# Performance work log

Measured on AMD Instinct MI355X. Metric: run time of the kernel, lower is better.

The kernel has to match this reference:

```python
import jax, jax.numpy as jnp
import numpy as np

V, E, HID, T, S = 50000, 512, 1024, 32, 4096
H = HID // 2  # per-direction hidden size


def setup_inputs() -> dict:
    key = jax.random.key(0)
    ks = jax.random.split(key, 16)
    f = lambda k, shape, s=0.1: (jax.random.normal(k, shape) * s).astype(jnp.float32)
    return {
        "input_ids": jax.random.randint(ks[0], (S,), 0, V),
        "target": jax.random.randint(ks[1], (S,), 0, T),
        "emb": f(ks[2], (V, E)),
        "wih_f": f(ks[3], (4 * H, E)),
        "whh_f": f(ks[4], (4 * H, H)),
        "b_f": f(ks[5], (4 * H,)),
        "wih_b": f(ks[6], (4 * H, E)),
        "whh_b": f(ks[7], (4 * H, H)),
        "b_b": f(ks[8], (4 * H,)),
        "lin_w": f(ks[9], (T, HID)),
        "lin_b": f(ks[10], (T,)),
        "start_trans": f(ks[11], (T,)),
        "end_trans": f(ks[12], (T,)),
        "trans": f(ks[13], (T, T)),
    }


def _lstm_dir(xp, whh):
    # xp: [S, 4H] precomputed input projections (x @ Wih^T + b_ih + b_hh)
    Hh = whh.shape[1]

    def step(carry, x_t):
        h, c = carry
        gates = x_t + whh @ h  # [4H]; PyTorch gate order: i, f, g, o
        i, fg, g, o = jnp.split(gates, 4)
        i = jax.nn.sigmoid(i)
        fg = jax.nn.sigmoid(fg)
        g = jnp.tanh(g)
        o = jax.nn.sigmoid(o)
        c = fg * c + i * g
        h = o * jnp.tanh(c)
        return (h, c), h

    init = (jnp.zeros((Hh,), xp.dtype), jnp.zeros((Hh,), xp.dtype))
    _, hs = jax.lax.scan(step, init, xp)
    return hs  # [S, H]


def reference(input_ids, target, emb, wih_f, whh_f, b_f, wih_b, whh_b, b_b,
              lin_w, lin_b, start_trans, end_trans, trans):
    x = emb[input_ids]  # [S, E]
    # bidirectional LSTM (batch of 1 sequence); dropout is identity (eval mode)
    h_f = _lstm_dir(x @ wih_f.T + b_f, whh_f)                # [S, H]
    h_b = _lstm_dir((x[::-1]) @ wih_b.T + b_b, whh_b)[::-1]  # [S, H]
    lstm_out = jnp.concatenate([h_f, h_b], axis=-1)          # [S, HID]
    em = lstm_out @ lin_w.T + lin_b                          # [S, T] emissions

    # CRF negative log-likelihood (mask all ones, batch=1, reduction='sum')
    idx = jnp.arange(em.shape[0])
    score = (start_trans[target[0]]
             + jnp.sum(em[idx, target])
             + jnp.sum(trans[target[:-1], target[1:]])
             + end_trans[target[-1]])

    alpha0 = start_trans + em[0]  # [T]

    def fstep(alpha, e_t):
        # logsumexp over previous tag: [T,1] + [T,T] -> [T]
        alpha = jax.scipy.special.logsumexp(alpha[:, None] + trans, axis=0) + e_t
        return alpha, None

    alpha, _ = jax.lax.scan(fstep, alpha0, em[1:])
    logZ = jax.scipy.special.logsumexp(alpha + end_trans)
    return logZ - score  # -log p(target | input), scalar
```

## Files before the change

### kernel.cpp

```cpp
#include <hip/hip_runtime.h>
#include <hip/hip_bf16.h>

#define S_LEN 4096
#define HID   512
#define E_DIM 512
#define G4    2048

__device__ __forceinline__ float fsig(float x) {
  return __fdividef(1.f, 1.f + __expf(-x));
}
__device__ __forceinline__ float ftanh_(float x) {
  return 1.f - __fdividef(2.f, __expf(2.f * x) + 1.f);
}
__device__ __forceinline__ unsigned int f2b(float f) {
  unsigned int x = __float_as_uint(f);
  return (x + 0x7FFFu + ((x >> 16) & 1u)) >> 16;
}
__device__ __forceinline__ float b2f(unsigned int b) {
  return __uint_as_float(b << 16);
}

__global__ __launch_bounds__(256) void proj_gemm(
    const int* __restrict__ ids, const float* __restrict__ emb,
    const float* __restrict__ wih_f, const float* __restrict__ wih_b,
    const float* __restrict__ b_f, const float* __restrict__ b_b,
    float* __restrict__ xp_f, float* __restrict__ xp_b)
{
  const int dir = blockIdx.z;
  const float* __restrict__ wih  = dir ? wih_b : wih_f;
  const float* __restrict__ bias = dir ? b_b : b_f;
  float* __restrict__ out = dir ? xp_b : xp_f;
  const int i0 = blockIdx.y * 128;
  const int j0 = blockIdx.x * 128;
  __shared__ __align__(16) float As[16 * 132];
  __shared__ __align__(16) float Bs[16 * 132];
  const int tid = threadIdx.x;
  const int ti = tid >> 4, tj = tid & 15;

  const int r0 = tid >> 2,        k40 = tid & 3;
  const int r1 = (tid + 256) >> 2, k41 = (tid + 256) & 3;
  const int id0 = ids[dir ? (S_LEN - 1 - (i0 + r0)) : (i0 + r0)];
  const int id1 = ids[dir ? (S_LEN - 1 - (i0 + r1)) : (i0 + r1)];
  const float* a0p = emb + (size_t)id0 * E_DIM + k40 * 4;
  const float* a1p = emb + (size_t)id1 * E_DIM + k41 * 4;
  const float* b0p = wih + (size_t)(j0 + r0) * E_DIM + k40 * 4;
  const float* b1p = wih + (size_t)(j0 + r1) * E_DIM + k41 * 4;

  float acc[8][8];
  #pragma unroll
  for (int x = 0; x < 8; ++x)
    #pragma unroll
    for (int y = 0; y < 8; ++y) acc[x][y] = 0.f;

  for (int k0 = 0; k0 < E_DIM; k0 += 16) {
    float4 va0 = *(const float4*)(a0p + k0);
    float4 va1 = *(const float4*)(a1p + k0);
    float4 vb0 = *(const float4*)(b0p + k0);
    float4 vb1 = *(const float4*)(b1p + k0);
    As[(k40*4+0)*132 + r0] = va0.x; As[(k40*4+1)*132 + r0] = va0.y;
    As[(k40*4+2)*132 + r0] = va0.z; As[(k40*4+3)*132 + r0] = va0.w;
    As[(k41*4+0)*132 + r1] = va1.x; As[(k41*4+1)*132 + r1] = va1.y;
    As[(k41*4+2)*132 + r1] = va1.z; As[(k41*4+3)*132 + r1] = va1.w;
    Bs[(k40*4+0)*132 + r0] = vb0.x; Bs[(k40*4+1)*132 + r0] = vb0.y;
    Bs[(k40*4+2)*132 + r0] = vb0.z; Bs[(k40*4+3)*132 + r0] = vb0.w;
    Bs[(k41*4+0)*132 + r1] = vb1.x; Bs[(k41*4+1)*132 + r1] = vb1.y;
    Bs[(k41*4+2)*132 + r1] = vb1.z; Bs[(k41*4+3)*132 + r1] = vb1.w;
    __syncthreads();
    const float4* As4 = (const float4*)As;
    const float4* Bs4 = (const float4*)Bs;
    #pragma unroll
    for (int k = 0; k < 16; ++k) {
      float4 al = As4[k*33 + ti];
      float4 ah = As4[k*33 + 16 + ti];
      float4 bl = Bs4[k*33 + tj];
      float4 bh = Bs4[k*33 + 16 + tj];
      float a[8] = {al.x, al.y, al.z, al.w, ah.x, ah.y, ah.z, ah.w};
      float b[8] = {bl.x, bl.y, bl.z, bl.w, bh.x, bh.y, bh.z, bh.w};
      #pragma unroll
      for (int x = 0; x < 8; ++x)
        #pragma unroll
        for (int y = 0; y < 8; ++y) acc[x][y] = fmaf(a[x], b[y], acc[x][y]);
    }
    __syncthreads();
  }
  float4 blo = *(const float4*)(bias + j0 + tj * 4);
  float4 bhi = *(const float4*)(bias + j0 + 64 + tj * 4);
  #pragma unroll
  for (int x = 0; x < 8; ++x) {
    int gi = i0 + ((x < 4) ? (ti * 4 + x) : (64 + ti * 4 + (x - 4)));
    float* orow = out + (size_t)gi * G4 + j0;
    float4 o0 = make_float4(acc[x][0] + blo.x, acc[x][1] + blo.y,
                            acc[x][2] + blo.z, acc[x][3] + blo.w);
    float4 o1 = make_float4(acc[x][4] + bhi.x, acc[x][5] + bhi.y,
                            acc[x][6] + bhi.z, acc[x][7] + bhi.w);
    *(float4*)(orow + tj * 4) = o0;
    *(float4*)(orow + 64 + tj * 4) = o1;
  }
}

__global__ __launch_bounds__(512, 2) void lstm_rec(
    const float* __restrict__ xp_f, const float* __restrict__ xp_b,
    const float* __restrict__ whh_f, const float* __restrict__ whh_b,
    float* __restrict__ hs, unsigned int* __restrict__ hslot)
{
  const int wg  = blockIdx.x;
  const int dir = wg >> 4, g = wg & 15;
  const float* __restrict__ xp  = dir ? xp_b  : xp_f;
  const float* __restrict__ whh = dir ? whh_b : whh_f;
  unsigned int* slot = hslot + dir * (4 * HID);
  const int tid  = threadIdx.x;
  const int lr   = tid >> 2;
  const int p    = tid & 3;
  const int gate = lr >> 5;
  const int uoff = lr & 31;
  const int U0   = g * 32;
  const int grow = gate * 512 + U0 + uoff;

  float w[128];
  {
    const float4* wp = (const float4*)(whh + (size_t)grow * HID + p * 128);
    #pragma unroll
    for (int u = 0; u < 32; ++u) {
      float4 v = wp[u];
      w[4*u] = v.x; w[4*u+1] = v.y; w[4*u+2] = v.z; w[4*u+3] = v.w;
    }
  }
  __shared__ __align__(16) float h_lds[528];
  __shared__ float gates_lds[128];
  for (int q = tid; q < 528; q += 512) h_lds[q] = 0.f;
  __syncthreads();

  float c = 0.f;
  float xpv = (p == 0) ? xp[grow] : 0.f;
  const int myslot_pos = (tid >> 7) * 132 + (tid & 127);

  for (int t = 0; t < S_LEN; ++t) {
    float a0 = 0.f, a1 = 0.f, a2 = 0.f, a3 = 0.f;
    const float4* hq = (const float4*)(h_lds + p * 132);
    #pragma unroll
    for (int u = 0; u < 32; ++u) {
      float4 hv = hq[u];
      a0 = fmaf(w[4*u],   hv.x, a0);
      a1 = fmaf(w[4*u+1], hv.y, a1);
      a2 = fmaf(w[4*u+2], hv.z, a2);
      a3 = fmaf(w[4*u+3], hv.w, a3);
    }
    float acc = (a0 + a1) + (a2 + a3);
    acc += __shfl_xor(acc, 1);
    acc += __shfl_xor(acc, 2);
    if (p == 0) gates_lds[lr] = acc + xpv;
    __syncthreads();
    if (p == 0 && t + 1 < S_LEN) xpv = xp[(size_t)(t + 1) * G4 + grow];
    const unsigned int tagn = (unsigned int)(t + 1);
    if (tid < 32) {
      float gi_ = gates_lds[tid];
      float gf_ = gates_lds[32 + tid];
      float gg_ = gates_lds[64 + tid];
      float go_ = gates_lds[96 + tid];
      float i_ = fsig(gi_), f_ = fsig(gf_), g2 = ftanh_(gg_), o_ = fsig(go_);
      c = f_ * c + i_ * g2;
      float h = o_ * ftanh_(c);
      const int trow = dir ? (S_LEN - 1 - t) : t;
      hs[(size_t)trow * 1024 + dir * HID + U0 + tid] = h;
      __hip_atomic_store(&slot[(tagn & 3) * HID + U0 + tid],
                         (tagn << 16) | f2b(h),
                         __ATOMIC_RELAXED, __HIP_MEMORY_SCOPE_AGENT);
    }
    if (t + 1 < S_LEN) {
      const unsigned int want = tagn << 16;
      unsigned int* pw = &slot[(tagn & 3) * HID + tid];
      unsigned int v; int guard = 0;
      for (;;) {
        v = __hip_atomic_load(pw, __ATOMIC_RELAXED, __HIP_MEMORY_SCOPE_AGENT);
        if ((v & 0xFFFF0000u) == want) break;
        if (++guard > (1 << 24)) break;
        __builtin_amdgcn_s_sleep(1);
      }
      h_lds[myslot_pos] = b2f(v & 0xFFFFu);
    }
    __syncthreads();
  }
}

__global__ __launch_bounds__(512) void emis_kernel(
    const float* __restrict__ hs, const float* __restrict__ lin_w,
    const float* __restrict__ lin_b, float* __restrict__ em)
{
  __shared__ float4 rows[4096];
  const int t0 = blockIdx.x * 16;
  const int tid = threadIdx.x;
  const float4* hs4 = (const float4*)(hs + (size_t)t0 * 1024);
  #pragma unroll
  for (int it = 0; it < 8; ++it) rows[it * 512 + tid] = hs4[it * 512 + tid];
  __syncthreads();
  const int r = tid >> 5, tag = tid & 31;
  const float4* w4 = (const float4*)(lin_w + (size_t)tag * 1024);
  float acc = 0.f;
  #pragma unroll 4
  for (int k = 0; k < 256; ++k) {
    float4 h = rows[r * 256 + k];
    float4 w = w4[k];
    acc += h.x * w.x + h.y * w.y + h.z * w.z + h.w * w.w;
  }
  em[(size_t)(t0 + r) * 32 + tag] = acc + lin_b[tag];
}

__global__ __launch_bounds__(64) void crf_kernel(
    const float* __restrict__ em, const int* __restrict__ tgt,
    const float* __restrict__ start_t, const float* __restrict__ end_t,
    const float* __restrict__ trans, float* __restrict__ out)
{
  const int lane = threadIdx.x;
  float se = 0.f;
  for (int t = lane; t < S_LEN; t += 64) {
    se += em[(size_t)t * 32 + tgt[t]];
    if (t + 1 < S_LEN) se += trans[tgt[t] * 32 + tgt[t + 1]];
  }
  #pragma unroll
  for (int m = 1; m < 64; m <<= 1) se += __shfl_xor(se, m);
  const float score = se + start_t[tgt[0]] + end_t[tgt[S_LEN - 1]];

  __shared__ __align__(16) float al[32];
  const int j = lane & 31, half = lane >> 5, i0 = half * 16;
  float tr[16];
  #pragma unroll
  for (int u = 0; u < 16; ++u) tr[u] = trans[(i0 + u) * 32 + j];
  if (lane < 32) al[j] = start_t[j] + em[j];
  __syncthreads();
  float ep = em[32 + j];
  for (int t = 1; t < S_LEN; ++t) {
    float epn = (t + 1 < S_LEN) ? em[(size_t)(t + 1) * 32 + j] : 0.f;
    float v[16];
    const float4* a4 = (const float4*)al;
    #pragma unroll
    for (int q = 0; q < 4; ++q) {
      float4 av = a4[half * 4 + q];
      v[4*q]   = av.x + tr[4*q];
      v[4*q+1] = av.y + tr[4*q+1];
      v[4*q+2] = av.z + tr[4*q+2];
      v[4*q+3] = av.w + tr[4*q+3];
    }
    float m = v[0];
    #pragma unroll
    for (int u = 1; u < 16; ++u) m = fmaxf(m, v[u]);
    m = fmaxf(m, __shfl_xor(m, 32));
    float s = 0.f;
    #pragma unroll
    for (int u = 0; u < 16; ++u) s += __expf(v[u] - m);
    s += __shfl_xor(s, 32);
    float an = m + __logf(s) + ep;
    __syncthreads();
    if (half == 0) al[j] = an;
    __syncthreads();
    ep = epn;
  }
  float x = (lane < 32) ? al[j] + end_t[j] : -1e30f;
  float mm = x;
  #pragma unroll
  for (int m2 = 1; m2 < 64; m2 <<= 1) mm = fmaxf(mm, __shfl_xor(mm, m2));
  float ss = (lane < 32) ? __expf(x - mm) : 0.f;
  #pragma unroll
  for (int m2 = 1; m2 < 64; m2 <<= 1) ss += __shfl_xor(ss, m2);
  if (lane == 0) out[0] = (mm + __logf(ss)) - score;
}

extern "C" void kernel_launch(void* const* d_in, const int* in_sizes, int n_in,
                              void* d_out, int out_size, void* d_ws, size_t ws_size,
                              hipStream_t stream) {
  const int*   ids   = (const int*)d_in[0];
  const int*   tgt   = (const int*)d_in[1];
  const float* emb   = (const float*)d_in[2];
  const float* wih_f = (const float*)d_in[3];
  const float* whh_f = (const float*)d_in[4];
  const float* b_f   = (const float*)d_in[5];
  const float* wih_b = (const float*)d_in[6];
  const float* whh_b = (const float*)d_in[7];
  const float* b_b   = (const float*)d_in[8];
  const float* lin_w = (const float*)d_in[9];
  const float* lin_b = (const float*)d_in[10];
  const float* st    = (const float*)d_in[11];
  const float* et    = (const float*)d_in[12];
  const float* trans = (const float*)d_in[13];

  float* xp_f = (float*)d_ws;
  float* xp_b = xp_f + (size_t)S_LEN * G4;
  float* hs   = xp_b + (size_t)S_LEN * G4;
  float* em   = hs   + (size_t)S_LEN * 1024;
  unsigned int* slot = (unsigned int*)(em + (size_t)S_LEN * 32);

  proj_gemm<<<dim3(16, 32, 2), dim3(256), 0, stream>>>(
      ids, emb, wih_f, wih_b, b_f, b_b, xp_f, xp_b);
  lstm_rec<<<dim3(32), dim3(512), 0, stream>>>(
      xp_f, xp_b, whh_f, whh_b, hs, slot);
  emis_kernel<<<dim3(256), dim3(512), 0, stream>>>(hs, lin_w, lin_b, em);
  crf_kernel<<<dim3(1), dim3(64), 0, stream>>>(em, tgt, st, et, trans,
                                               (float*)d_out);
}
```

Baseline: 9.258 ms.

## Cut LSTM step barriers and parallelize CRF forward via chunked log-semiring products

The LSTM recurrence now interleaves gate rows so each group of 16 threads owns one hidden unit. Gate activations are exchanged through wave shuffles instead of shared memory, and h is double-buffered so each timestep needs only one barrier. Each block writes its own units straight into LDS and spins only on remote units. The serial 4096-step CRF forward scan is split into a parallel pass that builds 16-step log-semiring transition products per chunk, plus a short 256-step serial combine that overlaps the gold-score reduction in a second wave. This trades extra CRF arithmetic for a much shorter serial dependency chain, and it changes the floating-point summation order.

```diff
diff --git a/kernel.cpp b/kernel.cpp
--- a/kernel.cpp
+++ b/kernel.cpp
@@ -6,12 +6,6 @@
 #define E_DIM 512
 #define G4    2048
 
-__device__ __forceinline__ float fsig(float x) {
-  return __fdividef(1.f, 1.f + __expf(-x));
-}
-__device__ __forceinline__ float ftanh_(float x) {
-  return 1.f - __fdividef(2.f, __expf(2.f * x) + 1.f);
-}
 __device__ __forceinline__ unsigned int f2b(float f) {
   unsigned int x = __float_as_uint(f);
   return (x + 0x7FFFu + ((x >> 16) & 1u)) >> 16;
@@ -109,12 +103,14 @@
   const float* __restrict__ whh = dir ? whh_b : whh_f;
   unsigned int* slot = hslot + dir * (4 * HID);
   const int tid  = threadIdx.x;
-  const int lr   = tid >> 2;
+  const int lane = tid & 63;
+  const int u_l  = tid >> 4;
+  const int gate = (tid >> 2) & 3;
   const int p    = tid & 3;
-  const int gate = lr >> 5;
-  const int uoff = lr & 31;
   const int U0   = g * 32;
-  const int grow = gate * 512 + U0 + uoff;
+  const int grow = gate * 512 + U0 + u_l;
+  const bool isg = (gate == 2);
+  const bool master = ((tid & 15) == 0);
 
   float w[128];
   {
@@ -125,18 +121,21 @@
       w[4*u] = v.x; w[4*u+1] = v.y; w[4*u+2] = v.z; w[4*u+3] = v.w;
     }
   }
-  __shared__ __align__(16) float h_lds[528];
-  __shared__ float gates_lds[128];
-  for (int q = tid; q < 528; q += 512) h_lds[q] = 0.f;
+  __shared__ __align__(16) float h_lds[2][544];
+  const int pollpos = (tid >> 7) * 136 + (tid & 127);
+  const int ownunit = U0 + u_l;
+  const int ownpos  = (ownunit >> 7) * 136 + (ownunit & 127);
+  h_lds[0][pollpos] = 0.f;
   __syncthreads();
 
   float c = 0.f;
-  float xpv = (p == 0) ? xp[grow] : 0.f;
-  const int myslot_pos = (tid >> 7) * 132 + (tid & 127);
+  float xpv = xp[grow];
+  int buf = 0;
+  const unsigned int rel = (unsigned int)(tid - U0);
 
   for (int t = 0; t < S_LEN; ++t) {
     float a0 = 0.f, a1 = 0.f, a2 = 0.f, a3 = 0.f;
-    const float4* hq = (const float4*)(h_lds + p * 132);
+    const float4* hq = (const float4*)(&h_lds[buf][p * 136]);
     #pragma unroll
     for (int u = 0; u < 32; ++u) {
       float4 hv = hq[u];
@@ -148,37 +147,47 @@
     float acc = (a0 + a1) + (a2 + a3);
     acc += __shfl_xor(acc, 1);
     acc += __shfl_xor(acc, 2);
-    if (p == 0) gates_lds[lr] = acc + xpv;
-    __syncthreads();
-    if (p == 0 && t + 1 < S_LEN) xpv = xp[(size_t)(t + 1) * G4 + grow];
+    float v = acc + xpv;
+    if (t + 1 < S_LEN) xpv = xp[(size_t)(t + 1) * G4 + grow];
+
+    float e = __expf(isg ? (v + v) : -v);
+    float r = __fdividef(1.f, 1.f + e);
+    float act = isg ? (1.f - 2.f * r) : r;
+    float a4  = __shfl(act, (lane + 4)  & 63);
+    float a8  = __shfl(act, (lane + 8)  & 63);
+    float a12 = __shfl(act, (lane + 12) & 63);
+
     const unsigned int tagn = (unsigned int)(t + 1);
-    if (tid < 32) {
-      float gi_ = gates_lds[tid];
-      float gf_ = gates_lds[32 + tid];
-      float gg_ = gates_lds[64 + tid];
-      float go_ = gates_lds[96 + tid];
-      float i_ = fsig(gi_), f_ = fsig(gf_), g2 = ftanh_(gg_), o_ = fsig(go_);
-      c = f_ * c + i_ * g2;
-      float h = o_ * ftanh_(c);
+    if (master) {
+      float i_ = act, f_ = a4, g_ = a8, o_ = a12;
+      c = f_ * c + i_ * g_;
+      float e2 = __expf(c + c);
+      float th = 1.f - 2.f * __fdividef(1.f, 1.f + e2);
+      float h = o_ * th;
+      unsigned int hb = f2b(h);
+      __hip_atomic_store(&slot[(tagn & 3) * HID + ownunit],
+                         (tagn << 16) | hb,
+                         __ATOMIC_RELAXED, __HIP_MEMORY_SCOPE_AGENT);
+      h_lds[buf ^ 1][ownpos] = b2f(hb);
       const int trow = dir ? (S_LEN - 1 - t) : t;
-      hs[(size_t)trow * 1024 + dir * HID + U0 + tid] = h;
-      __hip_atomic_store(&slot[(tagn & 3) * HID + U0 + tid],
-                         (tagn << 16) | f2b(h),
-                         __ATOMIC_RELAXED, __HIP_MEMORY_SCOPE_AGENT);
+      hs[(size_t)trow * 1024 + dir * HID + ownunit] = h;
     }
     if (t + 1 < S_LEN) {
-      const unsigned int want = tagn << 16;
-      unsigned int* pw = &slot[(tagn & 3) * HID + tid];
-      unsigned int v; int guard = 0;
-      for (;;) {
-        v = __hip_atomic_load(pw, __ATOMIC_RELAXED, __HIP_MEMORY_SCOPE_AGENT);
-        if ((v & 0xFFFF0000u) == want) break;
-        if (++guard > (1 << 24)) break;
-        __builtin_amdgcn_s_sleep(1);
+      if (rel >= 32u) {
+        const unsigned int want = tagn;
+        unsigned int* pw = &slot[(tagn & 3) * HID + tid];
+        unsigned int vv; int it = 0;
+        for (;;) {
+          vv = __hip_atomic_load(pw, __ATOMIC_RELAXED, __HIP_MEMORY_SCOPE_AGENT);
+          if ((vv >> 16) == want) break;
+          if (++it > 64) __builtin_amdgcn_s_sleep(1);
+          if (it > (1 << 22)) break;
+        }
+        h_lds[buf ^ 1][pollpos] = b2f(vv & 0xFFFFu);
       }
-      h_lds[myslot_pos] = b2f(v & 0xFFFFu);
-    }
-    __syncthreads();
+      __syncthreads();
+    }
+    buf ^= 1;
   }
 }
 
@@ -205,63 +214,112 @@
   em[(size_t)(t0 + r) * 32 + tag] = acc + lin_b[tag];
 }
 
-__global__ __launch_bounds__(64) void crf_kernel(
-    const float* __restrict__ em, const int* __restrict__ tgt,
-    const float* __restrict__ start_t, const float* __restrict__ end_t,
-    const float* __restrict__ trans, float* __restrict__ out)
-{
-  const int lane = threadIdx.x;
-  float se = 0.f;
-  for (int t = lane; t < S_LEN; t += 64) {
-    se += em[(size_t)t * 32 + tgt[t]];
-    if (t + 1 < S_LEN) se += trans[tgt[t] * 32 + tgt[t + 1]];
-  }
-  #pragma unroll
-  for (int m = 1; m < 64; m <<= 1) se += __shfl_xor(se, m);
-  const float score = se + start_t[tgt[0]] + end_t[tgt[S_LEN - 1]];
-
-  __shared__ __align__(16) float al[32];
-  const int j = lane & 31, half = lane >> 5, i0 = half * 16;
-  float tr[16];
-  #pragma unroll
-  for (int u = 0; u < 16; ++u) tr[u] = trans[(i0 + u) * 32 + j];
-  if (lane < 32) al[j] = start_t[j] + em[j];
+__global__ __launch_bounds__(1024) void crf_pass1(
+    const float* __restrict__ em, const float* __restrict__ trans,
+    float* __restrict__ Pt)
+{
+  __shared__ float tr[32 * 33];
+  __shared__ float bufA[32 * 33], bufB[32 * 33];
+  const int tid = threadIdx.x;
+  const int i = tid >> 5, j = tid & 31;
+  tr[i * 33 + j] = trans[i * 32 + j];
+  const int c = blockIdx.x;
+  const int t0 = (c == 0) ? 1 : c * 16;
+  const int t1 = c * 16 + 16;
+  bufA[i * 33 + j] = trans[i * 32 + j] + em[(size_t)t0 * 32 + j];
   __syncthreads();
-  float ep = em[32 + j];
-  for (int t = 1; t < S_LEN; ++t) {
-    float epn = (t + 1 < S_LEN) ? em[(size_t)(t + 1) * 32 + j] : 0.f;
-    float v[16];
-    const float4* a4 = (const float4*)al;
-    #pragma unroll
-    for (int q = 0; q < 4; ++q) {
-      float4 av = a4[half * 4 + q];
-      v[4*q]   = av.x + tr[4*q];
-      v[4*q+1] = av.y + tr[4*q+1];
-      v[4*q+2] = av.z + tr[4*q+2];
-      v[4*q+3] = av.w + tr[4*q+3];
-    }
-    float m = v[0];
-    #pragma unroll
-    for (int u = 1; u < 16; ++u) m = fmaxf(m, v[u]);
-    m = fmaxf(m, __shfl_xor(m, 32));
+
+  float* cur = bufA;
+  float* nxt = bufB;
+  for (int t = t0 + 1; t < t1; ++t) {
+    float m = -1e30f;
+    #pragma unroll
+    for (int k = 0; k < 32; ++k)
+      m = fmaxf(m, cur[i * 33 + k] + tr[k * 33 + j]);
     float s = 0.f;
     #pragma unroll
-    for (int u = 0; u < 16; ++u) s += __expf(v[u] - m);
-    s += __shfl_xor(s, 32);
-    float an = m + __logf(s) + ep;
+    for (int k = 0; k < 32; ++k)
+      s += __expf(cur[i * 33 + k] + tr[k * 33 + j] - m);
+    float nv = m + __logf(s) + em[(size_t)t * 32 + j];
+    nxt[i * 33 + j] = nv;
     __syncthreads();
-    if (half == 0) al[j] = an;
-    __syncthreads();
-    ep = epn;
-  }
-  float x = (lane < 32) ? al[j] + end_t[j] : -1e30f;
-  float mm = x;
-  #pragma unroll
-  for (int m2 = 1; m2 < 64; m2 <<= 1) mm = fmaxf(mm, __shfl_xor(mm, m2));
-  float ss = (lane < 32) ? __expf(x - mm) : 0.f;
-  #pragma unroll
-  for (int m2 = 1; m2 < 64; m2 <<= 1) ss += __shfl_xor(ss, m2);
-  if (lane == 0) out[0] = (mm + __logf(ss)) - score;
+    float* tmp = cur; cur = nxt; nxt = tmp;
+  }
+  Pt[(size_t)c * 1024 + tid] = cur[(tid & 31) * 33 + (tid >> 5)];
+}
+
+__global__ __launch_bounds__(128) void crf_pass2(
+    const float* __restrict__ em, const float* __restrict__ Pt,
+    const int* __restrict__ tgt, const float* __restrict__ st,
+    const float* __restrict__ et, const float* __restrict__ trans,
+    float* __restrict__ out)
+{
+  __shared__ float als[32];
+  __shared__ float gold[2];
+  const int tid = threadIdx.x;
+  const int lane = tid & 63;
+  const int wv = tid >> 6;
+
+  if (wv == 1) {
+    float se = 0.f;
+    for (int t = lane; t < S_LEN; t += 64) {
+      int tg = tgt[t];
+      se += em[(size_t)t * 32 + tg];
+      if (t + 1 < S_LEN) se += trans[tg * 32 + tgt[t + 1]];
+    }
+    #pragma unroll
+    for (int m = 1; m < 64; m <<= 1) se += __shfl_xor(se, m);
+    if (lane == 0) gold[0] = se + st[tgt[0]] + et[tgt[S_LEN - 1]];
+  } else {
+    const int jj = lane & 31;
+    float a = st[jj] + em[jj];
+    float4 P0, P1, P2, P3, P4, P5, P6, P7;
+    {
+      const float* pb = Pt + jj * 32;
+      P0 = *(const float4*)(pb +  0); P1 = *(const float4*)(pb +  4);
+      P2 = *(const float4*)(pb +  8); P3 = *(const float4*)(pb + 12);
+      P4 = *(const float4*)(pb + 16); P5 = *(const float4*)(pb + 20);
+      P6 = *(const float4*)(pb + 24); P7 = *(const float4*)(pb + 28);
+    }
+    for (int cc = 0; cc < 256; ++cc) {
+      float4 N0, N1, N2, N3, N4, N5, N6, N7;
+      if (cc < 255) {
+        const float* pb = Pt + (size_t)(cc + 1) * 1024 + jj * 32;
+        N0 = *(const float4*)(pb +  0); N1 = *(const float4*)(pb +  4);
+        N2 = *(const float4*)(pb +  8); N3 = *(const float4*)(pb + 12);
+        N4 = *(const float4*)(pb + 16); N5 = *(const float4*)(pb + 20);
+        N6 = *(const float4*)(pb + 24); N7 = *(const float4*)(pb + 28);
+      }
+      als[jj] = a;
+      float m = -1e30f;
+      #define MAXQ(Q, b) \
+        m = fmaxf(m, fmaxf(fmaxf(als[b+0] + Q.x, als[b+1] + Q.y), \
+                           fmaxf(als[b+2] + Q.z, als[b+3] + Q.w)));
+      MAXQ(P0, 0) MAXQ(P1, 4) MAXQ(P2, 8)  MAXQ(P3, 12)
+      MAXQ(P4,16) MAXQ(P5,20) MAXQ(P6,24)  MAXQ(P7,28)
+      float s = 0.f;
+      #define SUMQ(Q, b) \
+        s += __expf(als[b+0] + Q.x - m) + __expf(als[b+1] + Q.y - m) + \
+             __expf(als[b+2] + Q.z - m) + __expf(als[b+3] + Q.w - m);
+      SUMQ(P0, 0) SUMQ(P1, 4) SUMQ(P2, 8)  SUMQ(P3, 12)
+      SUMQ(P4,16) SUMQ(P5,20) SUMQ(P6,24)  SUMQ(P7,28)
+      #undef MAXQ
+      #undef SUMQ
+      a = m + __logf(s);
+      P0 = N0; P1 = N1; P2 = N2; P3 = N3;
+      P4 = N4; P5 = N5; P6 = N6; P7 = N7;
+    }
+    float x = (lane < 32) ? a + et[jj] : -1e30f;
+    float mm = x;
+    #pragma unroll
+    for (int m2 = 1; m2 < 64; m2 <<= 1) mm = fmaxf(mm, __shfl_xor(mm, m2));
+    float ss = (lane < 32) ? __expf(x - mm) : 0.f;
+    #pragma unroll
+    for (int m2 = 1; m2 < 64; m2 <<= 1) ss += __shfl_xor(ss, m2);
+    if (lane == 0) gold[1] = mm + __logf(ss);
+  }
+  __syncthreads();
+  if (tid == 0) out[0] = gold[1] - gold[0];
 }
 
 extern "C" void kernel_launch(void* const* d_in, const int* in_sizes, int n_in,
@@ -287,12 +345,14 @@
   float* hs   = xp_b + (size_t)S_LEN * G4;
   float* em   = hs   + (size_t)S_LEN * 1024;
   unsigned int* slot = (unsigned int*)(em + (size_t)S_LEN * 32);
+  float* Pt   = xp_f;
 
   proj_gemm<<<dim3(16, 32, 2), dim3(256), 0, stream>>>(
       ids, emb, wih_f, wih_b, b_f, b_b, xp_f, xp_b);
   lstm_rec<<<dim3(32), dim3(512), 0, stream>>>(
       xp_f, xp_b, whh_f, whh_b, hs, slot);
   emis_kernel<<<dim3(256), dim3(512), 0, stream>>>(hs, lin_w, lin_b, em);
-  crf_kernel<<<dim3(1), dim3(64), 0, stream>>>(em, tgt, st, et, trans,
+  crf_pass1<<<dim3(256), dim3(1024), 0, stream>>>(em, trans, Pt);
+  crf_pass2<<<dim3(1), dim3(128), 0, stream>>>(em, Pt, tgt, st, et, trans,
                                                (float*)d_out);
 }
```

Measured after the change: 8.078 ms. 1.15x faster.
